# Optimization experiments

Hardware: AMD Instinct MI355X
Metric: run time of the kernel (lower is better)

Reference implementation:

```python
import jax, jax.numpy as jnp
import numpy as np
import math

B, S, E = 4, 2048, 1024


def setup_inputs() -> dict:
    key = jax.random.key(0)
    ks = jax.random.split(key, 7)
    w_scale = 1.0 / math.sqrt(E)
    x = jax.random.normal(ks[0], (B, S, E), dtype=jnp.float32)
    Wq = jax.random.normal(ks[1], (E, E), dtype=jnp.float32) * w_scale
    bq = jax.random.normal(ks[2], (E,), dtype=jnp.float32) * 0.01
    Wk = jax.random.normal(ks[3], (E, E), dtype=jnp.float32) * w_scale
    bk = jax.random.normal(ks[4], (E,), dtype=jnp.float32) * 0.01
    Wv = jax.random.normal(ks[5], (E, E), dtype=jnp.float32) * w_scale
    bv = jax.random.normal(ks[6], (E,), dtype=jnp.float32) * 0.01
    # causal mask: True = attend, False = masked (mask == 0 -> -inf)
    mask = jnp.broadcast_to(jnp.tril(jnp.ones((S, S), dtype=bool)), (B, S, S))
    return {"x": x, "Wq": Wq, "bq": bq, "Wk": Wk, "bk": bk, "Wv": Wv, "bv": bv, "mask": mask}


def reference(x, Wq, bq, Wk, bk, Wv, bv, mask):
    # nn.Linear stores weight as [out, in]: y = x @ W.T + b
    Q = jnp.einsum("bse,oe->bso", x, Wq) + bq
    K = jnp.einsum("bse,oe->bso", x, Wk) + bk
    V = jnp.einsum("bse,oe->bso", x, Wv) + bv
    scale = math.sqrt(E)
    scores = jnp.einsum("bqe,bke->bqk", Q, K) / scale  # [B,S,S]
    scores = jnp.where(mask, scores, -jnp.inf)
    attn = jax.nn.softmax(scores, axis=-1)
    out = jnp.einsum("bqk,bke->bqe", attn, V)  # [B,S,E]
    return out
```

## Files before the change

kernel.cpp:

```cpp
#include <hip/hip_runtime.h>
#include <stdint.h>

typedef unsigned short u16;
typedef __attribute__((ext_vector_type(8))) short bf16x8;
typedef __attribute__((ext_vector_type(4))) float f32x4;

#define MFMA16(a, b, c) __builtin_amdgcn_mfma_f32_16x16x32_bf16((a), (b), (c), 0, 0, 0)

#define MASKVAL (-1.0e30f)

#define WAITV(N) asm volatile("s_waitcnt vmcnt(" #N ")" ::: "memory")
#define LGKM0()  asm volatile("s_waitcnt lgkmcnt(0)" ::: "memory")
#define SBAR()   __builtin_amdgcn_s_barrier()

__device__ __forceinline__ u16 f2bf(float f) {
  union { float f; uint32_t u; } v; v.f = f;
  uint32_t u = v.u;
  u += 0x7fffu + ((u >> 16) & 1u);
  return (u16)(u >> 16);
}
__device__ __forceinline__ void async16(const void* g, void* l) {
  __builtin_amdgcn_global_load_lds(
      (const __attribute__((address_space(1))) unsigned int*)g,
      (__attribute__((address_space(3))) unsigned int*)l, 16, 0, 0);
}

__global__ __launch_bounds__(256) void conv_kernel(
    const float* __restrict__ x,  const float* __restrict__ wq,
    const float* __restrict__ wk, const float* __restrict__ wv,
    u16* __restrict__ xb, u16* __restrict__ wb, int do_wv)
{
  const int NX = 1 << 20;
  const int NW = 1 << 17;
  const int total = NX + NW * (do_wv ? 3 : 2);
  for (int i = blockIdx.x * 256 + threadIdx.x; i < total; i += gridDim.x * 256) {
    const float* src; u16* dst;
    if (i < NX) {
      src = x + (size_t)i * 8;
      const int m = i >> 7, k8 = i & 127;
      dst = xb + (size_t)m * 2048 + 1024 + k8 * 8;
    } else {
      const int j = i - NX;
      const int wsel = j >> 17;
      const int jj = j & (NW - 1);
      const float* W = (wsel == 0) ? wq : (wsel == 1) ? wk : wv;
      const int zoff = (wsel == 0) ? 0 : (wsel == 1) ? (2 << 20) : (1 << 20);
      src = W + (size_t)jj * 8;
      dst = wb + zoff + jj * 8;
    }
    float4 f0 = *(const float4*)src;
    float4 f1 = *(const float4*)(src + 4);
    ushort4 h0, h1;
    h0.x = f2bf(f0.x); h0.y = f2bf(f0.y); h0.z = f2bf(f0.z); h0.w = f2bf(f0.w);
    h1.x = f2bf(f1.x); h1.y = f2bf(f1.y); h1.z = f2bf(f1.z); h1.w = f2bf(f1.w);
    *(ushort4*)dst = h0;
    *(ushort4*)(dst + 4) = h1;
  }
}

template <int BMODE>
__global__ __launch_bounds__(256) void gemm_kernel(
    const u16* __restrict__ xb,
    const u16* __restrict__ wb,
    const float* __restrict__ wv_f,
    const float* __restrict__ bq, const float* __restrict__ bk,
    const float* __restrict__ bv,
    u16* __restrict__ q_out, u16* __restrict__ vt_out, u16* __restrict__ k_out,
    int mode)
{
  __shared__ u16 lA[2][128 * 32];
  __shared__ u16 lB[2][128 * 32];

  const int flat = blockIdx.x;
  const int xcd = flat & 7, idx = flat >> 3;
  int n_g, mm, z;
  if (mode == 0)      { n_g = xcd * 3 + idx % 3;  mm = idx / 3;  z = n_g >> 3; }
  else if (mode == 1) { n_g = xcd * 2 + (idx & 1); mm = idx >> 1; z = (n_g < 8) ? 0 : 2; }
  else                { n_g = xcd;                 mm = idx;      z = 1; }
  const int m0 = mm * 128, n0 = (n_g & 7) * 128;

  const int tid = threadIdx.x, lane = tid & 63, w = tid >> 6;
  const int quad = lane >> 4, l15 = lane & 15;
  const int wr = (w >> 1) * 64, wc = (w & 1) * 64;

  const u16* wz = wb + ((size_t)z << 20);
  const float* bias = (z == 0) ? bq : (z == 1) ? bv : bk;

  const int sr  = lane >> 2;
  const int ssw = (lane >> 3) & 3;
  const int c16s = (lane & 3) ^ ssw;

  auto stageA = [&](int kk, int bbuf) {
    const int k0 = kk * 32;
#pragma unroll
    for (int i = 0; i < 2; ++i) {
      const int r = w * 32 + i * 16 + sr;
      async16(&xb[(size_t)(m0 + r) * 2048 + 1024 + k0 + c16s * 8],
              &lA[bbuf][w * 1024 + i * 512]);
    }
  };
  auto stageB = [&](int kk, int bbuf) {
    const int k0 = kk * 32;
#pragma unroll
    for (int i = 0; i < 2; ++i) {
      const int r = w * 32 + i * 16 + sr;
      async16(&wz[(size_t)(n0 + r) * 1024 + k0 + c16s * 8],
              &lB[bbuf][w * 1024 + i * 512]);
    }
  };

  float4 bfr[4];
  const int br = tid >> 1;
  const int bcb = (tid & 1) * 2;
  const int bs = (br >> 1) & 3;
  auto loadB = [&](int kk) {
    const float* p = &wv_f[(size_t)(n0 + br) * 1024 + kk * 32 + bcb * 8];
    bfr[0] = ((const float4*)p)[0];
    bfr[1] = ((const float4*)p)[1];
    bfr[2] = ((const float4*)p)[2];
    bfr[3] = ((const float4*)p)[3];
  };
  auto writeB = [&](int bbuf) {
    ushort4 h[4];
#pragma unroll
    for (int g = 0; g < 4; ++g) {
      h[g].x = f2bf(bfr[g].x); h[g].y = f2bf(bfr[g].y);
      h[g].z = f2bf(bfr[g].z); h[g].w = f2bf(bfr[g].w);
    }
    const int p0 = (bcb + 0) ^ bs, p1 = (bcb + 1) ^ bs;
    *(ushort4*)&lB[bbuf][br * 32 + p0 * 8]     = h[0];
    *(ushort4*)&lB[bbuf][br * 32 + p0 * 8 + 4] = h[1];
    *(ushort4*)&lB[bbuf][br * 32 + p1 * 8]     = h[2];
    *(ushort4*)&lB[bbuf][br * 32 + p1 * 8 + 4] = h[3];
  };

  f32x4 zero4 = {0.f, 0.f, 0.f, 0.f};
  f32x4 acc[4][4];
#pragma unroll
  for (int i = 0; i < 4; ++i)
#pragma unroll
    for (int j = 0; j < 4; ++j) acc[i][j] = zero4;

  if constexpr (BMODE == 0) {
    stageA(0, 0); stageB(0, 0);
  } else {
    stageA(0, 0); loadB(0); writeB(0);
  }

  const int fxor = (l15 >> 1) & 3;
  for (int kk = 0; kk < 32; ++kk) {
    const int bbuf = kk & 1;
    __syncthreads();
    if (kk + 1 < 32) {
      stageA(kk + 1, bbuf ^ 1);
      if constexpr (BMODE == 0) stageB(kk + 1, bbuf ^ 1);
      else loadB(kk + 1);
    }
    bf16x8 af[4], bw[4];
#pragma unroll
    for (int mf = 0; mf < 4; ++mf)
      af[mf] = *(const bf16x8*)
          &lA[bbuf][(wr + mf * 16 + l15) * 32 + (quad ^ fxor) * 8];
#pragma unroll
    for (int nf = 0; nf < 4; ++nf)
      bw[nf] = *(const bf16x8*)
          &lB[bbuf][(wc + nf * 16 + l15) * 32 + (quad ^ fxor) * 8];
    __builtin_amdgcn_s_setprio(1);
#pragma unroll
    for (int mf = 0; mf < 4; ++mf)
#pragma unroll
      for (int nf = 0; nf < 4; ++nf)
        acc[mf][nf] = MFMA16(af[mf], bw[nf], acc[mf][nf]);
    __builtin_amdgcn_s_setprio(0);
    if constexpr (BMODE == 1) {
      if (kk + 1 < 32) writeB(bbuf ^ 1);
    }
  }

  float bvv[4];
#pragma unroll
  for (int nf = 0; nf < 4; ++nf)
    bvv[nf] = bias[n0 + wc + nf * 16 + l15];

  if (z == 0) {
    const float qs = 0.03125f;
#pragma unroll
    for (int mf = 0; mf < 4; ++mf) {
#pragma unroll
      for (int nf = 0; nf < 4; ++nf) {
        const int n = n0 + wc + nf * 16 + l15;
#pragma unroll
        for (int r = 0; r < 4; ++r) {
          const int m = m0 + wr + mf * 16 + quad * 4 + r;
          q_out[(size_t)m * 2048 + n] = f2bf((acc[mf][nf][r] + bvv[nf]) * qs);
        }
      }
    }
  } else if (z == 1) {
#pragma unroll
    for (int mf = 0; mf < 4; ++mf) {
      const int mbase = m0 + wr + mf * 16 + quad * 4;
      const int bb = mbase >> 11;
      const int ss = mbase & 2047;
#pragma unroll
      for (int nf = 0; nf < 4; ++nf) {
        const int n = n0 + wc + nf * 16 + l15;
        ushort4 pk;
        pk.x = f2bf(acc[mf][nf][0] + bvv[nf]);
        pk.y = f2bf(acc[mf][nf][1] + bvv[nf]);
        pk.z = f2bf(acc[mf][nf][2] + bvv[nf]);
        pk.w = f2bf(acc[mf][nf][3] + bvv[nf]);
        *(ushort4*)&vt_out[((size_t)bb << 21) + (size_t)n * 2048 + ss] = pk;
      }
    }
  } else {
#pragma unroll
    for (int mf = 0; mf < 4; ++mf) {
#pragma unroll
      for (int nf = 0; nf < 4; ++nf) {
        const int n = n0 + wc + nf * 16 + l15;
#pragma unroll
        for (int r = 0; r < 4; ++r) {
          const int m = m0 + wr + mf * 16 + quad * 4 + r;
          k_out[(size_t)m * 1024 + n] = f2bf(acc[mf][nf][r] + bvv[nf]);
        }
      }
    }
  }
}

__global__ __launch_bounds__(512) void attn_kernel(
    const u16* __restrict__ Q, const u16* __restrict__ K,
    const u16* __restrict__ VT, float* out)
{
  constexpr int SLOT = 20480;
  __shared__ u16   ring[3][SLOT];
  __shared__ float sS[32 * 132];
  __shared__ u16   sP[32 * 136];
  __shared__ float sAlpha[32];
  __shared__ float sLinv[32];

  const int lin = blockIdx.x + ((int)blockIdx.y << 6);
  const int xcd = lin & 7;
  const int t = ((lin >> 3) << 1) | (xcd & 1);
  const int b = xcd >> 1;
  const int q0 = t * 32;
  const int tid = threadIdx.x, lane = tid & 63, w = tid >> 6;
  const int quad = lane >> 4, l15 = lane & 15;
  const u16* Qb  = Q  + ((size_t)b << 22);
  const u16* Kb  = K  + ((size_t)b << 21);
  const u16* VTb = VT + ((size_t)b << 21);
  float* outb = out + ((size_t)b << 21);

  const int sr = lane >> 4;
  const int sp = lane & 15;

  auto issueK = [&](int kv0, int e0, u16* slot) {
#pragma unroll
    for (int jj = 0; jj < 4; ++jj) {
      const int j = w * 4 + jj;
      const int r = j * 4 + sr;
      const int c16 = sp ^ (r & 15);
      async16(&Kb[(size_t)(kv0 + r) * 1024 + e0 + c16 * 8], slot + j * 512);
    }
  };
  auto issueV = [&](int kv0, int ck, u16* slot) {
#pragma unroll
    for (int jj = 0; jj < 4; ++jj) {
      const int j = w * 4 + jj;
      const int r = j * 4 + sr;
      const int c16 = sp ^ (r & 15);
      async16(&VTb[(size_t)(ck * 128 + r) * 2048 + kv0 + c16 * 8], slot + j * 512);
    }
  };
  auto issueQ = [&](int cq, u16* slot) {
    const int r = w * 4 + sr;
    const int c16 = sp ^ (r & 15);
    async16(&Qb[(size_t)(q0 + r) * 2048 + cq * 128 + c16 * 8],
            slot + 16384 + w * 512);
  };

  f32x4 zero4 = {0.f, 0.f, 0.f, 0.f};
  f32x4 accO[8][2];
#pragma unroll
  for (int c = 0; c < 8; ++c)
#pragma unroll
    for (int i = 0; i < 2; ++i) accO[c][i] = zero4;

  float m_i = MASKVAL, l_i = 0.f;
  const int srow = tid >> 4, slane = tid & 15;

  issueK(0, 0, ring[0]);   issueQ(0, ring[0]);
  issueK(0, 128, ring[1]); issueQ(1, ring[1]);
  int sl = 0, sl2 = 2;

  const int niter = q0 / 128 + 1;
  for (int it = 0; it < niter; ++it) {
    const int kv0 = it * 128;

    f32x4 accS[2];
    accS[0] = zero4; accS[1] = zero4;

#pragma unroll
    for (int c = 0; c < 8; ++c) {
      if (c < 7) { WAITV(5); } else { WAITV(4); }
      SBAR();
      u16* dst = ring[sl2];
      if (c < 6)      { issueK(kv0, (c + 2) * 128, dst); issueQ(c + 2, dst); }
      else if (c == 6) issueV(kv0, 0, dst);
      else             issueV(kv0, 1, dst);
      const u16* bufK = ring[sl];
      const u16* bufQ = ring[sl] + 16384;
      __builtin_amdgcn_s_setprio(1);
#pragma unroll
      for (int ks = 0; ks < 4; ++ks) {
        const int cc = ks * 4 + quad;
        bf16x8 a0 = *(const bf16x8*)&bufQ[l15 * 128 + (cc ^ l15) * 8];
        bf16x8 a1 = *(const bf16x8*)&bufQ[(16 + l15) * 128 + (cc ^ l15) * 8];
        bf16x8 b0 = *(const bf16x8*)&bufK[(w * 16 + l15) * 128 + (cc ^ l15) * 8];
        accS[0] = MFMA16(a0, b0, accS[0]);
        accS[1] = MFMA16(a1, b0, accS[1]);
      }
      __builtin_amdgcn_s_setprio(0);
      sl  = (sl  == 2) ? 0 : sl  + 1;
      sl2 = (sl2 == 2) ? 0 : sl2 + 1;
    }

#pragma unroll
    for (int mf = 0; mf < 2; ++mf)
#pragma unroll
      for (int r = 0; r < 4; ++r) {
        const int row = mf * 16 + quad * 4 + r;
        const int col = w * 16 + l15;
        sS[row * 132 + col] = (kv0 + col <= q0 + row) ? accS[mf][r] : MASKVAL;
      }
    LGKM0();
    SBAR();

    {
      float v[8];
      float4 t0 = *(const float4*)&sS[srow * 132 + slane * 8 + 0];
      float4 t1 = *(const float4*)&sS[srow * 132 + slane * 8 + 4];
      v[0]=t0.x; v[1]=t0.y; v[2]=t0.z; v[3]=t0.w;
      v[4]=t1.x; v[5]=t1.y; v[6]=t1.z; v[7]=t1.w;
      float mx = v[0];
#pragma unroll
      for (int j = 1; j < 8; ++j) mx = fmaxf(mx, v[j]);
#pragma unroll
      for (int d = 1; d < 16; d <<= 1) mx = fmaxf(mx, __shfl_xor(mx, d, 64));
      const float mnew  = fmaxf(m_i, mx);
      const float alpha = __expf(m_i - mnew);
      float sum = 0.f;
      u16 pb[8];
#pragma unroll
      for (int j = 0; j < 8; ++j) {
        const float p = __expf(v[j] - mnew);
        pb[j] = f2bf(p);
        union { uint32_t u; float f; } pv; pv.u = ((uint32_t)pb[j]) << 16;
        sum += pv.f;
      }
      ushort4 pk0, pk1;
      pk0.x = pb[0]; pk0.y = pb[1]; pk0.z = pb[2]; pk0.w = pb[3];
      pk1.x = pb[4]; pk1.y = pb[5]; pk1.z = pb[6]; pk1.w = pb[7];
      *(ushort4*)&sP[srow * 136 + slane * 8 + 0] = pk0;
      *(ushort4*)&sP[srow * 136 + slane * 8 + 4] = pk1;
#pragma unroll
      for (int d = 1; d < 16; d <<= 1) sum += __shfl_xor(sum, d, 64);
      l_i = l_i * alpha + sum;
      m_i = mnew;
      if (slane == 0) sAlpha[srow] = alpha;
      if (it == niter - 1 && slane == 0) sLinv[srow] = 1.0f / l_i;
    }
    LGKM0();
    SBAR();

    float av[2][4];
#pragma unroll
    for (int mf = 0; mf < 2; ++mf)
#pragma unroll
      for (int r = 0; r < 4; ++r)
        av[mf][r] = sAlpha[mf * 16 + quad * 4 + r];
#pragma unroll
    for (int c = 0; c < 8; ++c)
#pragma unroll
      for (int mf = 0; mf < 2; ++mf)
#pragma unroll
        for (int r = 0; r < 4; ++r) accO[c][mf][r] *= av[mf][r];

    bf16x8 pf0[4], pf1[4];
#pragma unroll
    for (int ks = 0; ks < 4; ++ks) {
      const int cc = ks * 4 + quad;
      pf0[ks] = *(const bf16x8*)&sP[l15 * 136 + cc * 8];
      pf1[ks] = *(const bf16x8*)&sP[(16 + l15) * 136 + cc * 8];
    }

#pragma unroll
    for (int k = 0; k < 8; ++k) {
      if (k < 7)                 { WAITV(4); }
      else if (it + 1 < niter)   { WAITV(5); }
      else                       { WAITV(0); }
      SBAR();
      u16* dst = ring[sl2];
      if (k < 6) issueV(kv0, k + 2, dst);
      else if (it + 1 < niter) {
        issueK(kv0 + 128, (k - 6) * 128, dst);
        issueQ(k - 6, dst);
      }
      const u16* bufV = ring[sl];
      __builtin_amdgcn_s_setprio(1);
#pragma unroll
      for (int ks = 0; ks < 4; ++ks) {
        const int cc = ks * 4 + quad;
        bf16x8 v0 = *(const bf16x8*)&bufV[(w * 16 + l15) * 128 + (cc ^ l15) * 8];
        accO[k][0] = MFMA16(pf0[ks], v0, accO[k][0]);
        accO[k][1] = MFMA16(pf1[ks], v0, accO[k][1]);
      }
      __builtin_amdgcn_s_setprio(0);
      sl  = (sl  == 2) ? 0 : sl  + 1;
      sl2 = (sl2 == 2) ? 0 : sl2 + 1;
    }
  }

  float lv[2][4];
#pragma unroll
  for (int mf = 0; mf < 2; ++mf)
#pragma unroll
    for (int r = 0; r < 4; ++r)
      lv[mf][r] = sLinv[mf * 16 + quad * 4 + r];
#pragma unroll
  for (int c = 0; c < 8; ++c)
#pragma unroll
    for (int mf = 0; mf < 2; ++mf) {
      const int col = c * 128 + w * 16 + l15;
#pragma unroll
      for (int r = 0; r < 4; ++r) {
        const int row = q0 + mf * 16 + quad * 4 + r;
        outb[(size_t)row * 1024 + col] = accO[c][mf][r] * lv[mf][r];
      }
    }
}

extern "C" void kernel_launch(void* const* d_in, const int* in_sizes, int n_in,
                              void* d_out, int out_size, void* d_ws, size_t ws_size,
                              hipStream_t stream) {
  (void)in_sizes; (void)n_in; (void)out_size;
  const float* x  = (const float*)d_in[0];
  const float* Wq = (const float*)d_in[1];
  const float* bq = (const float*)d_in[2];
  const float* Wk = (const float*)d_in[3];
  const float* bk = (const float*)d_in[4];
  const float* Wv = (const float*)d_in[5];
  const float* bv = (const float*)d_in[6];

  u16* qbuf = (u16*)d_out;
  u16* vtw  = (u16*)d_in[7];
  u16* kw   = (u16*)d_ws;

  const bool ws_big = ws_size >= (size_t)22 * 1024 * 1024;
  u16* wb = ws_big ? (u16*)d_ws + (8u << 20) : (u16*)d_in[7];

  conv_kernel<<<dim3(2048), 256, 0, stream>>>(x, Wq, Wk, Wv, qbuf, wb,
                                              ws_big ? 1 : 0);
  if (ws_big) {
    gemm_kernel<0><<<dim3(1536), 256, 0, stream>>>(
        qbuf, wb, Wv, bq, bk, bv, qbuf, vtw, kw, 0);
  } else {
    gemm_kernel<0><<<dim3(1024), 256, 0, stream>>>(
        qbuf, wb, Wv, bq, bk, bv, qbuf, vtw, kw, 1);
    gemm_kernel<1><<<dim3(512), 256, 0, stream>>>(
        qbuf, wb, Wv, bq, bk, bv, qbuf, vtw, kw, 2);
  }

  attn_kernel<<<dim3(64, 4), 512, 0, stream>>>(qbuf, kw, vtw, (float*)d_out);
}
```

Before: 414.0 us.

## Enlarge attention query tile to 64 rows and triple-buffer projection GEMM

The attention kernel now processes 64 query rows per block instead of 32. It arranges 8 waves as a 2x4 grid, does the softmax in registers with cross-wave max/sum exchange through small shared arrays, and double-buffers Q in its own LDS area. This halves K/V reloads per query and removes the sS score staging, at the cost of more registers and fewer blocks (128 instead of 256 on a large GPU). The projection GEMM moves from double to triple-buffered async loads with explicit vmcnt waits, and the V path with inline fp32 conversion is split into its own kernel.

```diff
diff --git a/kernel.cpp b/kernel.cpp
--- a/kernel.cpp
+++ b/kernel.cpp
@@ -58,25 +58,22 @@
   }
 }
 
-template <int BMODE>
 __global__ __launch_bounds__(256) void gemm_kernel(
     const u16* __restrict__ xb,
     const u16* __restrict__ wb,
-    const float* __restrict__ wv_f,
     const float* __restrict__ bq, const float* __restrict__ bk,
     const float* __restrict__ bv,
     u16* __restrict__ q_out, u16* __restrict__ vt_out, u16* __restrict__ k_out,
     int mode)
 {
-  __shared__ u16 lA[2][128 * 32];
-  __shared__ u16 lB[2][128 * 32];
+  __shared__ u16 lA[3][128 * 32];
+  __shared__ u16 lB[3][128 * 32];
 
   const int flat = blockIdx.x;
   const int xcd = flat & 7, idx = flat >> 3;
   int n_g, mm, z;
   if (mode == 0)      { n_g = xcd * 3 + idx % 3;  mm = idx / 3;  z = n_g >> 3; }
-  else if (mode == 1) { n_g = xcd * 2 + (idx & 1); mm = idx >> 1; z = (n_g < 8) ? 0 : 2; }
-  else                { n_g = xcd;                 mm = idx;      z = 1; }
+  else                { n_g = xcd * 2 + (idx & 1); mm = idx >> 1; z = (n_g < 8) ? 0 : 2; }
   const int m0 = mm * 128, n0 = (n_g & 7) * 128;
 
   const int tid = threadIdx.x, lane = tid & 63, w = tid >> 6;
@@ -109,6 +106,125 @@
     }
   };
 
+  f32x4 zero4 = {0.f, 0.f, 0.f, 0.f};
+  f32x4 acc[4][4];
+#pragma unroll
+  for (int i = 0; i < 4; ++i)
+#pragma unroll
+    for (int j = 0; j < 4; ++j) acc[i][j] = zero4;
+
+  stageA(0, 0); stageB(0, 0);
+  stageA(1, 1); stageB(1, 1);
+
+  const int fxor = (l15 >> 1) & 3;
+  int cur = 0;
+  for (int kk = 0; kk < 32; ++kk) {
+    if (kk < 31) { WAITV(4); } else { WAITV(0); }
+    SBAR();
+    if (kk + 2 < 32) {
+      int nx = cur + 2; if (nx >= 3) nx -= 3;
+      stageA(kk + 2, nx);
+      stageB(kk + 2, nx);
+    }
+    bf16x8 af[4], bw[4];
+#pragma unroll
+    for (int mf = 0; mf < 4; ++mf)
+      af[mf] = *(const bf16x8*)
+          &lA[cur][(wr + mf * 16 + l15) * 32 + (quad ^ fxor) * 8];
+#pragma unroll
+    for (int nf = 0; nf < 4; ++nf)
+      bw[nf] = *(const bf16x8*)
+          &lB[cur][(wc + nf * 16 + l15) * 32 + (quad ^ fxor) * 8];
+    __builtin_amdgcn_s_setprio(1);
+#pragma unroll
+    for (int mf = 0; mf < 4; ++mf)
+#pragma unroll
+      for (int nf = 0; nf < 4; ++nf)
+        acc[mf][nf] = MFMA16(af[mf], bw[nf], acc[mf][nf]);
+    __builtin_amdgcn_s_setprio(0);
+    cur = (cur == 2) ? 0 : cur + 1;
+  }
+
+  float bvv[4];
+#pragma unroll
+  for (int nf = 0; nf < 4; ++nf)
+    bvv[nf] = bias[n0 + wc + nf * 16 + l15];
+
+  if (z == 0) {
+    const float qs = 0.03125f;
+#pragma unroll
+    for (int mf = 0; mf < 4; ++mf) {
+#pragma unroll
+      for (int nf = 0; nf < 4; ++nf) {
+        const int n = n0 + wc + nf * 16 + l15;
+#pragma unroll
+        for (int r = 0; r < 4; ++r) {
+          const int m = m0 + wr + mf * 16 + quad * 4 + r;
+          q_out[(size_t)m * 2048 + n] = f2bf((acc[mf][nf][r] + bvv[nf]) * qs);
+        }
+      }
+    }
+  } else if (z == 1) {
+#pragma unroll
+    for (int mf = 0; mf < 4; ++mf) {
+      const int mbase = m0 + wr + mf * 16 + quad * 4;
+      const int bb = mbase >> 11;
+      const int ss = mbase & 2047;
+#pragma unroll
+      for (int nf = 0; nf < 4; ++nf) {
+        const int n = n0 + wc + nf * 16 + l15;
+        ushort4 pk;
+        pk.x = f2bf(acc[mf][nf][0] + bvv[nf]);
+        pk.y = f2bf(acc[mf][nf][1] + bvv[nf]);
+        pk.z = f2bf(acc[mf][nf][2] + bvv[nf]);
+        pk.w = f2bf(acc[mf][nf][3] + bvv[nf]);
+        *(ushort4*)&vt_out[((size_t)bb << 21) + (size_t)n * 2048 + ss] = pk;
+      }
+    }
+  } else {
+#pragma unroll
+    for (int mf = 0; mf < 4; ++mf) {
+#pragma unroll
+      for (int nf = 0; nf < 4; ++nf) {
+        const int n = n0 + wc + nf * 16 + l15;
+#pragma unroll
+        for (int r = 0; r < 4; ++r) {
+          const int m = m0 + wr + mf * 16 + quad * 4 + r;
+          k_out[(size_t)m * 1024 + n] = f2bf(acc[mf][nf][r] + bvv[nf]);
+        }
+      }
+    }
+  }
+}
+
+__global__ __launch_bounds__(256) void gemm_v_kernel(
+    const u16* __restrict__ xb, const float* __restrict__ wv_f,
+    const float* __restrict__ bv, u16* __restrict__ vt_out)
+{
+  __shared__ u16 lA[2][128 * 32];
+  __shared__ u16 lB[2][128 * 32];
+
+  const int flat = blockIdx.x;
+  const int xcd = flat & 7, idx = flat >> 3;
+  const int m0 = idx * 128, n0 = xcd * 128;
+
+  const int tid = threadIdx.x, lane = tid & 63, w = tid >> 6;
+  const int quad = lane >> 4, l15 = lane & 15;
+  const int wr = (w >> 1) * 64, wc = (w & 1) * 64;
+
+  const int sr  = lane >> 2;
+  const int ssw = (lane >> 3) & 3;
+  const int c16s = (lane & 3) ^ ssw;
+
+  auto stageA = [&](int kk, int bbuf) {
+    const int k0 = kk * 32;
+#pragma unroll
+    for (int i = 0; i < 2; ++i) {
+      const int r = w * 32 + i * 16 + sr;
+      async16(&xb[(size_t)(m0 + r) * 2048 + 1024 + k0 + c16s * 8],
+              &lA[bbuf][w * 1024 + i * 512]);
+    }
+  };
   float4 bfr[4];
   const int br = tid >> 1;
   const int bcb = (tid & 1) * 2;
@@ -141,21 +257,13 @@
 #pragma unroll
     for (int j = 0; j < 4; ++j) acc[i][j] = zero4;
 
-  if constexpr (BMODE == 0) {
-    stageA(0, 0); stageB(0, 0);
-  } else {
-    stageA(0, 0); loadB(0); writeB(0);
-  }
+  stageA(0, 0); loadB(0); writeB(0);
 
   const int fxor = (l15 >> 1) & 3;
   for (int kk = 0; kk < 32; ++kk) {
     const int bbuf = kk & 1;
     __syncthreads();
-    if (kk + 1 < 32) {
-      stageA(kk + 1, bbuf ^ 1);
-      if constexpr (BMODE == 0) stageB(kk + 1, bbuf ^ 1);
-      else loadB(kk + 1);
-    }
+    if (kk + 1 < 32) { stageA(kk + 1, bbuf ^ 1); loadB(kk + 1); }
     bf16x8 af[4], bw[4];
 #pragma unroll
     for (int mf = 0; mf < 4; ++mf)
@@ -165,66 +273,32 @@
     for (int nf = 0; nf < 4; ++nf)
       bw[nf] = *(const bf16x8*)
           &lB[bbuf][(wc + nf * 16 + l15) * 32 + (quad ^ fxor) * 8];
-    __builtin_amdgcn_s_setprio(1);
 #pragma unroll
     for (int mf = 0; mf < 4; ++mf)
 #pragma unroll
       for (int nf = 0; nf < 4; ++nf)
         acc[mf][nf] = MFMA16(af[mf], bw[nf], acc[mf][nf]);
-    __builtin_amdgcn_s_setprio(0);
-    if constexpr (BMODE == 1) {
-      if (kk + 1 < 32) writeB(bbuf ^ 1);
-    }
+    if (kk + 1 < 32) writeB(bbuf ^ 1);
   }
 
   float bvv[4];
 #pragma unroll
   for (int nf = 0; nf < 4; ++nf)
-    bvv[nf] = bias[n0 + wc + nf * 16 + l15];
-
-  if (z == 0) {
-    const float qs = 0.03125f;
-#pragma unroll
-    for (int mf = 0; mf < 4; ++mf) {
-#pragma unroll
-      for (int nf = 0; nf < 4; ++nf) {
-        const int n = n0 + wc + nf * 16 + l15;
-#pragma unroll
-        for (int r = 0; r < 4; ++r) {
-          const int m = m0 + wr + mf * 16 + quad * 4 + r;
-          q_out[(size_t)m * 2048 + n] = f2bf((acc[mf][nf][r] + bvv[nf]) * qs);
-        }
-      }
-    }
-  } else if (z == 1) {
-#pragma unroll
-    for (int mf = 0; mf < 4; ++mf) {
-      const int mbase = m0 + wr + mf * 16 + quad * 4;
-      const int bb = mbase >> 11;
-      const int ss = mbase & 2047;
-#pragma unroll
-      for (int nf = 0; nf < 4; ++nf) {
-        const int n = n0 + wc + nf * 16 + l15;
-        ushort4 pk;
-        pk.x = f2bf(acc[mf][nf][0] + bvv[nf]);
-        pk.y = f2bf(acc[mf][nf][1] + bvv[nf]);
-        pk.z = f2bf(acc[mf][nf][2] + bvv[nf]);
-        pk.w = f2bf(acc[mf][nf][3] + bvv[nf]);
-        *(ushort4*)&vt_out[((size_t)bb << 21) + (size_t)n * 2048 + ss] = pk;
-      }
-    }
-  } else {
-#pragma unroll
-    for (int mf = 0; mf < 4; ++mf) {
-#pragma unroll
-      for (int nf = 0; nf < 4; ++nf) {
-        const int n = n0 + wc + nf * 16 + l15;
-#pragma unroll
-        for (int r = 0; r < 4; ++r) {
-          const int m = m0 + wr + mf * 16 + quad * 4 + r;
-          k_out[(size_t)m * 1024 + n] = f2bf(acc[mf][nf][r] + bvv[nf]);
-        }
-      }
+    bvv[nf] = bv[n0 + wc + nf * 16 + l15];
+#pragma unroll
+  for (int mf = 0; mf < 4; ++mf) {
+    const int mbase = m0 + wr + mf * 16 + quad * 4;
+    const int bb = mbase >> 11;
+    const int ss = mbase & 2047;
+#pragma unroll
+    for (int nf = 0; nf < 4; ++nf) {
+      const int n = n0 + wc + nf * 16 + l15;
+      ushort4 pk;
+      pk.x = f2bf(acc[mf][nf][0] + bvv[nf]);
+      pk.y = f2bf(acc[mf][nf][1] + bvv[nf]);
+      pk.z = f2bf(acc[mf][nf][2] + bvv[nf]);
+      pk.w = f2bf(acc[mf][nf][3] + bvv[nf]);
+      *(ushort4*)&vt_out[((size_t)bb << 21) + (size_t)n * 2048 + ss] = pk;
     }
   }
 }
@@ -233,20 +307,21 @@
     const u16* __restrict__ Q, const u16* __restrict__ K,
     const u16* __restrict__ VT, float* out)
 {
-  constexpr int SLOT = 20480;
-  __shared__ u16   ring[3][SLOT];
-  __shared__ float sS[32 * 132];
-  __shared__ u16   sP[32 * 136];
-  __shared__ float sAlpha[32];
-  __shared__ float sLinv[32];
-
-  const int lin = blockIdx.x + ((int)blockIdx.y << 6);
+  __shared__ u16   ring[3][16384];
+  __shared__ u16   qd[2][8192];
+  __shared__ u16   sP[64 * 136];
+  __shared__ float pmaxb[64][4];
+  __shared__ float psumb[64][4];
+
+  const int lin = blockIdx.x + ((int)blockIdx.y << 5);
   const int xcd = lin & 7;
   const int t = ((lin >> 3) << 1) | (xcd & 1);
   const int b = xcd >> 1;
-  const int q0 = t * 32;
+  const int q0 = t * 64;
   const int tid = threadIdx.x, lane = tid & 63, w = tid >> 6;
   const int quad = lane >> 4, l15 = lane & 15;
+  const int wq = w >> 2;
+  const int wk = w & 3;
   const u16* Qb  = Q  + ((size_t)b << 22);
   const u16* Kb  = K  + ((size_t)b << 21);
   const u16* VTb = VT + ((size_t)b << 21);
@@ -255,71 +330,88 @@
   const int sr = lane >> 4;
   const int sp = lane & 15;
 
-  auto issueK = [&](int kv0, int e0, u16* slot) {
+  auto issueK = [&](int kv0_, int e0, u16* slot) {
 #pragma unroll
     for (int jj = 0; jj < 4; ++jj) {
       const int j = w * 4 + jj;
       const int r = j * 4 + sr;
       const int c16 = sp ^ (r & 15);
-      async16(&Kb[(size_t)(kv0 + r) * 1024 + e0 + c16 * 8], slot + j * 512);
-    }
-  };
-  auto issueV = [&](int kv0, int ck, u16* slot) {
+      async16(&Kb[(size_t)(kv0_ + r) * 1024 + e0 + c16 * 8], slot + j * 512);
+    }
+  };
+  auto issueV = [&](int kv0_, int ck, u16* slot) {
 #pragma unroll
     for (int jj = 0; jj < 4; ++jj) {
       const int j = w * 4 + jj;
       const int r = j * 4 + sr;
       const int c16 = sp ^ (r & 15);
-      async16(&VTb[(size_t)(ck * 128 + r) * 2048 + kv0 + c16 * 8], slot + j * 512);
-    }
-  };
-  auto issueQ = [&](int cq, u16* slot) {
-    const int r = w * 4 + sr;
-    const int c16 = sp ^ (r & 15);
-    async16(&Qb[(size_t)(q0 + r) * 2048 + cq * 128 + c16 * 8],
-            slot + 16384 + w * 512);
+      async16(&VTb[(size_t)(ck * 128 + r) * 2048 + kv0_ + c16 * 8], slot + j * 512);
+    }
+  };
+  auto issueQ = [&](int cq) {
+#pragma unroll
+    for (int jj = 0; jj < 2; ++jj) {
+      const int j = w * 2 + jj;
+      const int r = j * 4 + sr;
+      const int c16 = sp ^ (r & 15);
+      async16(&Qb[(size_t)(q0 + r) * 2048 + cq * 128 + c16 * 8],
+              &qd[cq & 1][j * 512]);
+    }
   };
 
   f32x4 zero4 = {0.f, 0.f, 0.f, 0.f};
-  f32x4 accO[8][2];
+  f32x4 accO[8][2][2];
 #pragma unroll
   for (int c = 0; c < 8; ++c)
 #pragma unroll
-    for (int i = 0; i < 2; ++i) accO[c][i] = zero4;
-
-  float m_i = MASKVAL, l_i = 0.f;
-  const int srow = tid >> 4, slane = tid & 15;
-
-  issueK(0, 0, ring[0]);   issueQ(0, ring[0]);
-  issueK(0, 128, ring[1]); issueQ(1, ring[1]);
+    for (int i = 0; i < 2; ++i)
+#pragma unroll
+      for (int j = 0; j < 2; ++j) accO[c][i][j] = zero4;
+
+  float m_i[2][4], l_i[2][4];
+#pragma unroll
+  for (int mf = 0; mf < 2; ++mf)
+#pragma unroll
+    for (int rr = 0; rr < 4; ++rr) { m_i[mf][rr] = MASKVAL; l_i[mf][rr] = 0.f; }
+
+  issueQ(0);
+  issueK(0, 0, ring[0]);
+  issueK(0, 128, ring[1]);
   int sl = 0, sl2 = 2;
 
   const int niter = q0 / 128 + 1;
   for (int it = 0; it < niter; ++it) {
     const int kv0 = it * 128;
 
-    f32x4 accS[2];
-    accS[0] = zero4; accS[1] = zero4;
+    f32x4 accS[2][2];
+#pragma unroll
+    for (int i = 0; i < 2; ++i)
+#pragma unroll
+      for (int j = 0; j < 2; ++j) accS[i][j] = zero4;
 
 #pragma unroll
     for (int c = 0; c < 8; ++c) {
-      if (c < 7) { WAITV(5); } else { WAITV(4); }
+      WAITV(4);
       SBAR();
+      issueQ((c + 1) & 7);
       u16* dst = ring[sl2];
-      if (c < 6)      { issueK(kv0, (c + 2) * 128, dst); issueQ(c + 2, dst); }
+      if (c < 6)       issueK(kv0, (c + 2) * 128, dst);
       else if (c == 6) issueV(kv0, 0, dst);
       else             issueV(kv0, 1, dst);
       const u16* bufK = ring[sl];
-      const u16* bufQ = ring[sl] + 16384;
+      const u16* bufQ = qd[c & 1];
       __builtin_amdgcn_s_setprio(1);
 #pragma unroll
       for (int ks = 0; ks < 4; ++ks) {
         const int cc = ks * 4 + quad;
-        bf16x8 a0 = *(const bf16x8*)&bufQ[l15 * 128 + (cc ^ l15) * 8];
-        bf16x8 a1 = *(const bf16x8*)&bufQ[(16 + l15) * 128 + (cc ^ l15) * 8];
-        bf16x8 b0 = *(const bf16x8*)&bufK[(w * 16 + l15) * 128 + (cc ^ l15) * 8];
-        accS[0] = MFMA16(a0, b0, accS[0]);
-        accS[1] = MFMA16(a1, b0, accS[1]);
+        bf16x8 a0 = *(const bf16x8*)&bufQ[(wq * 32 + l15) * 128 + (cc ^ l15) * 8];
+        bf16x8 a1 = *(const bf16x8*)&bufQ[(wq * 32 + 16 + l15) * 128 + (cc ^ l15) * 8];
+        bf16x8 b0 = *(const bf16x8*)&bufK[(wk * 32 + l15) * 128 + (cc ^ l15) * 8];
+        bf16x8 b1 = *(const bf16x8*)&bufK[(wk * 32 + 16 + l15) * 128 + (cc ^ l15) * 8];
+        accS[0][0] = MFMA16(a0, b0, accS[0][0]);
+        accS[0][1] = MFMA16(a0, b1, accS[0][1]);
+        accS[1][0] = MFMA16(a1, b0, accS[1][0]);
+        accS[1][1] = MFMA16(a1, b1, accS[1][1]);
       }
       __builtin_amdgcn_s_setprio(0);
       sl  = (sl  == 2) ? 0 : sl  + 1;
@@ -329,92 +421,88 @@
 #pragma unroll
     for (int mf = 0; mf < 2; ++mf)
 #pragma unroll
-      for (int r = 0; r < 4; ++r) {
-        const int row = mf * 16 + quad * 4 + r;
-        const int col = w * 16 + l15;
-        sS[row * 132 + col] = (kv0 + col <= q0 + row) ? accS[mf][r] : MASKVAL;
+      for (int rr = 0; rr < 4; ++rr) {
+        const int R = wq * 32 + mf * 16 + quad * 4 + rr;
+        const int gr = q0 + R;
+        const float s0 = (kv0 + wk * 32 + l15      <= gr) ? accS[mf][0][rr] : MASKVAL;
+        const float s1 = (kv0 + wk * 32 + 16 + l15 <= gr) ? accS[mf][1][rr] : MASKVAL;
+        float m = fmaxf(s0, s1);
+#pragma unroll
+        for (int d = 1; d < 16; d <<= 1) m = fmaxf(m, __shfl_xor(m, d, 64));
+        if (l15 == 0) pmaxb[R][wk] = m;
       }
     LGKM0();
     SBAR();
 
-    {
-      float v[8];
-      float4 t0 = *(const float4*)&sS[srow * 132 + slane * 8 + 0];
-      float4 t1 = *(const float4*)&sS[srow * 132 + slane * 8 + 4];
-      v[0]=t0.x; v[1]=t0.y; v[2]=t0.z; v[3]=t0.w;
-      v[4]=t1.x; v[5]=t1.y; v[6]=t1.z; v[7]=t1.w;
-      float mx = v[0];
-#pragma unroll
-      for (int j = 1; j < 8; ++j) mx = fmaxf(mx, v[j]);
-#pragma unroll
-      for (int d = 1; d < 16; d <<= 1) mx = fmaxf(mx, __shfl_xor(mx, d, 64));
-      const float mnew  = fmaxf(m_i, mx);
-      const float alpha = __expf(m_i - mnew);
-      float sum = 0.f;
-      u16 pb[8];
-#pragma unroll
-      for (int j = 0; j < 8; ++j) {
-        const float p = __expf(v[j] - mnew);
-        pb[j] = f2bf(p);
-        union { uint32_t u; float f; } pv; pv.u = ((uint32_t)pb[j]) << 16;
-        sum += pv.f;
-      }
-      ushort4 pk0, pk1;
-      pk0.x = pb[0]; pk0.y = pb[1]; pk0.z = pb[2]; pk0.w = pb[3];
-      pk1.x = pb[4]; pk1.y = pb[5]; pk1.z = pb[6]; pk1.w = pb[7];
-      *(ushort4*)&sP[srow * 136 + slane * 8 + 0] = pk0;
-      *(ushort4*)&sP[srow * 136 + slane * 8 + 4] = pk1;
-#pragma unroll
-      for (int d = 1; d < 16; d <<= 1) sum += __shfl_xor(sum, d, 64);
-      l_i = l_i * alpha + sum;
-      m_i = mnew;
-      if (slane == 0) sAlpha[srow] = alpha;
-      if (it == niter - 1 && slane == 0) sLinv[srow] = 1.0f / l_i;
-    }
+    float alpha_[2][4];
+#pragma unroll
+    for (int mf = 0; mf < 2; ++mf)
+#pragma unroll
+      for (int rr = 0; rr < 4; ++rr) {
+        const int R = wq * 32 + mf * 16 + quad * 4 + rr;
+        const int gr = q0 + R;
+        const float4 pm4 = *(const float4*)&pmaxb[R][0];
+        const float mrow = fmaxf(fmaxf(pm4.x, pm4.y), fmaxf(pm4.z, pm4.w));
+        const float mnew = fmaxf(m_i[mf][rr], mrow);
+        alpha_[mf][rr] = __expf(m_i[mf][rr] - mnew);
+        m_i[mf][rr] = mnew;
+        float s = 0.f;
+#pragma unroll
+        for (int nf = 0; nf < 2; ++nf) {
+          const int C = wk * 32 + nf * 16 + l15;
+          const float p = (kv0 + C <= gr) ? __expf(accS[mf][nf][rr] - mnew) : 0.f;
+          const u16 pb = f2bf(p);
+          sP[R * 136 + C] = pb;
+          union { uint32_t u; float f; } pv; pv.u = ((uint32_t)pb) << 16;
+          s += pv.f;
+        }
+#pragma unroll
+        for (int d = 1; d < 16; d <<= 1) s += __shfl_xor(s, d, 64);
+        if (l15 == 0) psumb[R][wk] = s;
+      }
     LGKM0();
     SBAR();
 
-    float av[2][4];
 #pragma unroll
     for (int mf = 0; mf < 2; ++mf)
 #pragma unroll
-      for (int r = 0; r < 4; ++r)
-        av[mf][r] = sAlpha[mf * 16 + quad * 4 + r];
-#pragma unroll
-    for (int c = 0; c < 8; ++c)
+      for (int rr = 0; rr < 4; ++rr) {
+        const int R = wq * 32 + mf * 16 + quad * 4 + rr;
+        const float4 ps4 = *(const float4*)&psumb[R][0];
+        l_i[mf][rr] = l_i[mf][rr] * alpha_[mf][rr] + (ps4.x + ps4.y + ps4.z + ps4.w);
+      }
+#pragma unroll
+    for (int cA = 0; cA < 8; ++cA)
 #pragma unroll
       for (int mf = 0; mf < 2; ++mf)
 #pragma unroll
-        for (int r = 0; r < 4; ++r) accO[c][mf][r] *= av[mf][r];
-
-    bf16x8 pf0[4], pf1[4];
-#pragma unroll
-    for (int ks = 0; ks < 4; ++ks) {
-      const int cc = ks * 4 + quad;
-      pf0[ks] = *(const bf16x8*)&sP[l15 * 136 + cc * 8];
-      pf1[ks] = *(const bf16x8*)&sP[(16 + l15) * 136 + cc * 8];
-    }
+        for (int nf = 0; nf < 2; ++nf)
+#pragma unroll
+          for (int rr = 0; rr < 4; ++rr)
+            accO[cA][mf][nf][rr] *= alpha_[mf][rr];
 
 #pragma unroll
     for (int k = 0; k < 8; ++k) {
-      if (k < 7)                 { WAITV(4); }
-      else if (it + 1 < niter)   { WAITV(5); }
-      else                       { WAITV(0); }
+      if (k == 0)                          { WAITV(6); }
+      else if (k < 7 || it + 1 < niter)    { WAITV(4); }
+      else                                 { WAITV(0); }
       SBAR();
       u16* dst = ring[sl2];
       if (k < 6) issueV(kv0, k + 2, dst);
-      else if (it + 1 < niter) {
-        issueK(kv0 + 128, (k - 6) * 128, dst);
-        issueQ(k - 6, dst);
-      }
+      else if (it + 1 < niter) issueK(kv0 + 128, (k - 6) * 128, dst);
       const u16* bufV = ring[sl];
       __builtin_amdgcn_s_setprio(1);
 #pragma unroll
       for (int ks = 0; ks < 4; ++ks) {
         const int cc = ks * 4 + quad;
-        bf16x8 v0 = *(const bf16x8*)&bufV[(w * 16 + l15) * 128 + (cc ^ l15) * 8];
-        accO[k][0] = MFMA16(pf0[ks], v0, accO[k][0]);
-        accO[k][1] = MFMA16(pf1[ks], v0, accO[k][1]);
+        bf16x8 p0 = *(const bf16x8*)&sP[(wq * 32 + l15) * 136 + cc * 8];
+        bf16x8 p1 = *(const bf16x8*)&sP[(wq * 32 + 16 + l15) * 136 + cc * 8];
+        bf16x8 v0 = *(const bf16x8*)&bufV[(wk * 32 + l15) * 128 + (cc ^ l15) * 8];
+        bf16x8 v1 = *(const bf16x8*)&bufV[(wk * 32 + 16 + l15) * 128 + (cc ^ l15) * 8];
+        accO[k][0][0] = MFMA16(p0, v0, accO[k][0][0]);
+        accO[k][0][1] = MFMA16(p0, v1, accO[k][0][1]);
+        accO[k][1][0] = MFMA16(p1, v0, accO[k][1][0]);
+        accO[k][1][1] = MFMA16(p1, v1, accO[k][1][1]);
       }
       __builtin_amdgcn_s_setprio(0);
       sl  = (sl  == 2) ? 0 : sl  + 1;
@@ -422,23 +510,24 @@
     }
   }
 
-  float lv[2][4];
+  float linv[2][4];
 #pragma unroll
   for (int mf = 0; mf < 2; ++mf)
 #pragma unroll
-    for (int r = 0; r < 4; ++r)
-      lv[mf][r] = sLinv[mf * 16 + quad * 4 + r];
+    for (int rr = 0; rr < 4; ++rr) linv[mf][rr] = 1.0f / l_i[mf][rr];
 #pragma unroll
   for (int c = 0; c < 8; ++c)
 #pragma unroll
-    for (int mf = 0; mf < 2; ++mf) {
-      const int col = c * 128 + w * 16 + l15;
-#pragma unroll
-      for (int r = 0; r < 4; ++r) {
-        const int row = q0 + mf * 16 + quad * 4 + r;
-        outb[(size_t)row * 1024 + col] = accO[c][mf][r] * lv[mf][r];
-      }
-    }
+    for (int mf = 0; mf < 2; ++mf)
+#pragma unroll
+      for (int nf = 0; nf < 2; ++nf) {
+        const int col = c * 128 + wk * 32 + nf * 16 + l15;
+#pragma unroll
+        for (int rr = 0; rr < 4; ++rr) {
+          const int row = q0 + wq * 32 + mf * 16 + quad * 4 + rr;
+          outb[(size_t)row * 1024 + col] = accO[c][mf][nf][rr] * linv[mf][rr];
+        }
+      }
 }
 
 extern "C" void kernel_launch(void* const* d_in, const int* in_sizes, int n_in,
@@ -463,14 +552,13 @@
   conv_kernel<<<dim3(2048), 256, 0, stream>>>(x, Wq, Wk, Wv, qbuf, wb,
                                               ws_big ? 1 : 0);
   if (ws_big) {
-    gemm_kernel<0><<<dim3(1536), 256, 0, stream>>>(
-        qbuf, wb, Wv, bq, bk, bv, qbuf, vtw, kw, 0);
+    gemm_kernel<<<dim3(1536), 256, 0, stream>>>(
+        qbuf, wb, bq, bk, bv, qbuf, vtw, kw, 0);
   } else {
-    gemm_kernel<0><<<dim3(1024), 256, 0, stream>>>(
-        qbuf, wb, Wv, bq, bk, bv, qbuf, vtw, kw, 1);
-    gemm_kernel<1><<<dim3(512), 256, 0, stream>>>(
-        qbuf, wb, Wv, bq, bk, bv, qbuf, vtw, kw, 2);
-  }
-
-  attn_kernel<<<dim3(64, 4), 512, 0, stream>>>(qbuf, kw, vtw, (float*)d_out);
-}
+    gemm_kernel<<<dim3(1024), 256, 0, stream>>>(
+        qbuf, wb, bq, bk, bv, qbuf, vtw, kw, 1);
+    gemm_v_kernel<<<dim3(512), 256, 0, stream>>>(qbuf, Wv, bv, vtw);
+  }
+
+  attn_kernel<<<dim3(32, 4), 512, 0, stream>>>(qbuf, kw, vtw, (float*)d_out);
+}
```

New measurement: 691.5 us. 1.67x slower.

## Replace QKV projection GEMM with 256x256-tile 8-wave ping-pong pipelined kernel

Applied to the files above, without the earlier changes.

The 128x128 tile, 4-wave QKV GEMM is replaced by a 512-thread kernel. It computes 256x256 output tiles with a K step of 64 and double-buffered half-tiles in LDS. Global-to-LDS async loads are interleaved with MFMA phases under barriers and explicit vmcnt waits. The larger tile raises arithmetic intensity and cuts block count, at the cost of more registers and LDS, fewer blocks per CU, and wave-quantization risk. The small-workspace fallback keeps a separate V GEMM kernel that converts Wv on the fly.

```diff
diff --git a/kernel.cpp b/kernel.cpp
--- a/kernel.cpp
+++ b/kernel.cpp
@@ -58,33 +58,292 @@
   }
 }
 
-template <int BMODE>
-__global__ __launch_bounds__(256) void gemm_kernel(
+__global__ __launch_bounds__(512) void gemm8_kernel(
     const u16* __restrict__ xb,
     const u16* __restrict__ wb,
-    const float* __restrict__ wv_f,
     const float* __restrict__ bq, const float* __restrict__ bk,
     const float* __restrict__ bv,
     u16* __restrict__ q_out, u16* __restrict__ vt_out, u16* __restrict__ k_out,
-    int mode)
+    int np)
+{
+  __shared__ u16 lA[2][2][128 * 64];
+  __shared__ u16 lB[2][2][128 * 64];
+
+  const int flat = blockIdx.x;
+  const int xcd = flat & 7, idx = flat >> 3;
+  int n_g, mm;
+  if (np == 12) { n_g = (xcd & 3) * 3 + idx % 3; mm = (xcd >> 2) * 16 + idx / 3; }
+  else          { n_g = xcd;                     mm = idx; }
+  const int z = (np == 12) ? (n_g >> 2) : ((n_g >> 2) ? 2 : 0);
+  const int m0 = mm * 256;
+  const int n0loc = (n_g & 3) * 256;
+  const u16* wz = wb + ((size_t)z << 20);
+  const float* bias = (z == 0) ? bq : (z == 1) ? bv : bk;
+
+  const int tid = threadIdx.x, lane = tid & 63, w = tid >> 6;
+  const int quad = lane >> 4, l15 = lane & 15;
+  const int wm = w >> 2, wn = w & 3;
+
+  const int srow = lane >> 3;
+  const int schk = (lane & 7) ^ srow;
+
+  auto stageA = [&](int d, int h, int kt) {
+#pragma unroll
+    for (int i = 0; i < 2; ++i) {
+      const int rr = w * 16 + i * 8;
+      async16(&xb[(size_t)(m0 + h * 128 + rr + srow) * 2048 + 1024 + kt * 64 + schk * 8],
+              &lA[d][h][rr * 64]);
+    }
+  };
+  auto stageB = [&](int d, int h, int kt) {
+#pragma unroll
+    for (int i = 0; i < 2; ++i) {
+      const int rr = w * 16 + i * 8;
+      async16(&wz[(size_t)(n0loc + h * 128 + rr + srow) * 1024 + kt * 64 + schk * 8],
+              &lB[d][h][rr * 64]);
+    }
+  };
+
+  f32x4 zero4 = {0.f, 0.f, 0.f, 0.f};
+  f32x4 acc[8][4];
+#pragma unroll
+  for (int i = 0; i < 8; ++i)
+#pragma unroll
+    for (int j = 0; j < 4; ++j) acc[i][j] = zero4;
+
+  auto rdA = [&](int d, int mf, int ks) -> bf16x8 {
+    const int hr = mf * 16 + l15;
+    return *(const bf16x8*)&lA[d][wm][hr * 64 + (((ks << 2) + quad) ^ (l15 & 7)) * 8];
+  };
+  auto rdB = [&](int d, int nf, int ks) -> bf16x8 {
+    const int hr = (wn & 1) * 64 + nf * 16 + l15;
+    return *(const bf16x8*)&lB[d][wn >> 1][hr * 64 + (((ks << 2) + quad) ^ (l15 & 7)) * 8];
+  };
+
+  stageA(0, 0, 0); stageA(0, 1, 0);
+  stageB(0, 0, 0); stageB(0, 1, 0);
+  stageA(1, 0, 1); stageB(1, 1, 1);
+  WAITV(0);
+  SBAR();
+
+  bf16x8 a[4][2], b[2][2];
+  for (int i = 0; i < 8; ++i) {
+    const int k1 = 2 * i + 1, k2 = 2 * i + 2, k3 = 2 * i + 3;
+    const bool more = (i < 7);
+
+#pragma unroll
+    for (int mf = 0; mf < 4; ++mf)
+#pragma unroll
+      for (int ks = 0; ks < 2; ++ks) a[mf][ks] = rdA(0, mf, ks);
+#pragma unroll
+    for (int nf = 0; nf < 2; ++nf)
+#pragma unroll
+      for (int ks = 0; ks < 2; ++ks) b[nf][ks] = rdB(0, nf, ks);
+    stageA(1, 1, k1);
+    SBAR();
+    __builtin_amdgcn_s_setprio(1);
+#pragma unroll
+    for (int mf = 0; mf < 4; ++mf)
+#pragma unroll
+      for (int nf = 0; nf < 2; ++nf)
+#pragma unroll
+        for (int ks = 0; ks < 2; ++ks)
+          acc[mf][nf] = MFMA16(a[mf][ks], b[nf][ks], acc[mf][nf]);
+    __builtin_amdgcn_s_setprio(0);
+    SBAR();
+
+#pragma unroll
+    for (int nf = 0; nf < 2; ++nf)
+#pragma unroll
+      for (int ks = 0; ks < 2; ++ks) b[nf][ks] = rdB(0, 2 + nf, ks);
+    stageB(1, 0, k1);
+    SBAR();
+    __builtin_amdgcn_s_setprio(1);
+#pragma unroll
+    for (int mf = 0; mf < 4; ++mf)
+#pragma unroll
+      for (int nf = 0; nf < 2; ++nf)
+#pragma unroll
+        for (int ks = 0; ks < 2; ++ks)
+          acc[mf][2 + nf] = MFMA16(a[mf][ks], b[nf][ks], acc[mf][2 + nf]);
+    __builtin_amdgcn_s_setprio(0);
+    SBAR();
+
+#pragma unroll
+    for (int mf = 0; mf < 4; ++mf)
+#pragma unroll
+      for (int ks = 0; ks < 2; ++ks) a[mf][ks] = rdA(0, 4 + mf, ks);
+    if (more) stageA(0, 0, k2);
+    SBAR();
+    __builtin_amdgcn_s_setprio(1);
+#pragma unroll
+    for (int mf = 0; mf < 4; ++mf)
+#pragma unroll
+      for (int nf = 0; nf < 2; ++nf)
+#pragma unroll
+        for (int ks = 0; ks < 2; ++ks)
+          acc[4 + mf][2 + nf] = MFMA16(a[mf][ks], b[nf][ks], acc[4 + mf][2 + nf]);
+    __builtin_amdgcn_s_setprio(0);
+    SBAR();
+
+#pragma unroll
+    for (int nf = 0; nf < 2; ++nf)
+#pragma unroll
+      for (int ks = 0; ks < 2; ++ks) b[nf][ks] = rdB(0, nf, ks);
+    if (more) stageB(0, 1, k2);
+    SBAR();
+    __builtin_amdgcn_s_setprio(1);
+#pragma unroll
+    for (int mf = 0; mf < 4; ++mf)
+#pragma unroll
+      for (int nf = 0; nf < 2; ++nf)
+#pragma unroll
+        for (int ks = 0; ks < 2; ++ks)
+          acc[4 + mf][nf] = MFMA16(a[mf][ks], b[nf][ks], acc[4 + mf][nf]);
+    __builtin_amdgcn_s_setprio(0);
+    if (more) { WAITV(4); } else { WAITV(0); }
+    SBAR();
+
+#pragma unroll
+    for (int mf = 0; mf < 4; ++mf)
+#pragma unroll
+      for (int ks = 0; ks < 2; ++ks) a[mf][ks] = rdA(1, mf, ks);
+#pragma unroll
+    for (int nf = 0; nf < 2; ++nf)
+#pragma unroll
+      for (int ks = 0; ks < 2; ++ks) b[nf][ks] = rdB(1, nf, ks);
+    if (more) stageA(0, 1, k2);
+    SBAR();
+    __builtin_amdgcn_s_setprio(1);
+#pragma unroll
+    for (int mf = 0; mf < 4; ++mf)
+#pragma unroll
+      for (int nf = 0; nf < 2; ++nf)
+#pragma unroll
+        for (int ks = 0; ks < 2; ++ks)
+          acc[mf][nf] = MFMA16(a[mf][ks], b[nf][ks], acc[mf][nf]);
+    __builtin_amdgcn_s_setprio(0);
+    SBAR();
+
+#pragma unroll
+    for (int nf = 0; nf < 2; ++nf)
+#pragma unroll
+      for (int ks = 0; ks < 2; ++ks) b[nf][ks] = rdB(1, 2 + nf, ks);
+    if (more) stageB(0, 0, k2);
+    SBAR();
+    __builtin_amdgcn_s_setprio(1);
+#pragma unroll
+    for (int mf = 0; mf < 4; ++mf)
+#pragma unroll
+      for (int nf = 0; nf < 2; ++nf)
+#pragma unroll
+        for (int ks = 0; ks < 2; ++ks)
+          acc[mf][2 + nf] = MFMA16(a[mf][ks], b[nf][ks], acc[mf][2 + nf]);
+    __builtin_amdgcn_s_setprio(0);
+    SBAR();
+
+#pragma unroll
+    for (int mf = 0; mf < 4; ++mf)
+#pragma unroll
+      for (int ks = 0; ks < 2; ++ks) a[mf][ks] = rdA(1, 4 + mf, ks);
+    if (more) stageA(1, 0, k3);
+    SBAR();
+    __builtin_amdgcn_s_setprio(1);
+#pragma unroll
+    for (int mf = 0; mf < 4; ++mf)
+#pragma unroll
+      for (int nf = 0; nf < 2; ++nf)
+#pragma unroll
+        for (int ks = 0; ks < 2; ++ks)
+          acc[4 + mf][2 + nf] = MFMA16(a[mf][ks], b[nf][ks], acc[4 + mf][2 + nf]);
+    __builtin_amdgcn_s_setprio(0);
+    SBAR();
+
+#pragma unroll
+    for (int nf = 0; nf < 2; ++nf)
+#pragma unroll
+      for (int ks = 0; ks < 2; ++ks) b[nf][ks] = rdB(1, nf, ks);
+    if (more) stageB(1, 1, k3);
+    SBAR();
+    __builtin_amdgcn_s_setprio(1);
+#pragma unroll
+    for (int mf = 0; mf < 4; ++mf)
+#pragma unroll
+      for (int nf = 0; nf < 2; ++nf)
+#pragma unroll
+        for (int ks = 0; ks < 2; ++ks)
+          acc[4 + mf][nf] = MFMA16(a[mf][ks], b[nf][ks], acc[4 + mf][nf]);
+    __builtin_amdgcn_s_setprio(0);
+    if (more) { WAITV(4); }
+    SBAR();
+  }
+
+  float bvv[4];
+#pragma unroll
+  for (int nf = 0; nf < 4; ++nf)
+    bvv[nf] = bias[n0loc + wn * 64 + nf * 16 + l15];
+
+  if (z == 0) {
+    const float qs = 0.03125f;
+#pragma unroll
+    for (int mf = 0; mf < 8; ++mf) {
+#pragma unroll
+      for (int nf = 0; nf < 4; ++nf) {
+        const int n = n0loc + wn * 64 + nf * 16 + l15;
+#pragma unroll
+        for (int rr = 0; rr < 4; ++rr) {
+          const int m = m0 + wm * 128 + mf * 16 + quad * 4 + rr;
+          q_out[(size_t)m * 2048 + n] = f2bf((acc[mf][nf][rr] + bvv[nf]) * qs);
+        }
+      }
+    }
+  } else if (z == 1) {
+#pragma unroll
+    for (int mf = 0; mf < 8; ++mf) {
+      const int mbase = m0 + wm * 128 + mf * 16 + quad * 4;
+      const int bb = mbase >> 11;
+      const int ss = mbase & 2047;
+#pragma unroll
+      for (int nf = 0; nf < 4; ++nf) {
+        const int n = n0loc + wn * 64 + nf * 16 + l15;
+        ushort4 pk;
+        pk.x = f2bf(acc[mf][nf][0] + bvv[nf]);
+        pk.y = f2bf(acc[mf][nf][1] + bvv[nf]);
+        pk.z = f2bf(acc[mf][nf][2] + bvv[nf]);
+        pk.w = f2bf(acc[mf][nf][3] + bvv[nf]);
+        *(ushort4*)&vt_out[((size_t)bb << 21) + (size_t)n * 2048 + ss] = pk;
+      }
+    }
+  } else {
+#pragma unroll
+    for (int mf = 0; mf < 8; ++mf) {
+#pragma unroll
+      for (int nf = 0; nf < 4; ++nf) {
+        const int n = n0loc + wn * 64 + nf * 16 + l15;
+#pragma unroll
+        for (int rr = 0; rr < 4; ++rr) {
+          const int m = m0 + wm * 128 + mf * 16 + quad * 4 + rr;
+          k_out[(size_t)m * 1024 + n] = f2bf(acc[mf][nf][rr] + bvv[nf]);
+        }
+      }
+    }
+  }
+}
+
+__global__ __launch_bounds__(256) void gemm_v_kernel(
+    const u16* __restrict__ xb, const float* __restrict__ wv_f,
+    const float* __restrict__ bv, u16* __restrict__ vt_out)
 {
   __shared__ u16 lA[2][128 * 32];
   __shared__ u16 lB[2][128 * 32];
 
   const int flat = blockIdx.x;
   const int xcd = flat & 7, idx = flat >> 3;
-  int n_g, mm, z;
-  if (mode == 0)      { n_g = xcd * 3 + idx % 3;  mm = idx / 3;  z = n_g >> 3; }
-  else if (mode == 1) { n_g = xcd * 2 + (idx & 1); mm = idx >> 1; z = (n_g < 8) ? 0 : 2; }
-  else                { n_g = xcd;                 mm = idx;      z = 1; }
-  const int m0 = mm * 128, n0 = (n_g & 7) * 128;
+  const int m0 = idx * 128, n0 = xcd * 128;
 
   const int tid = threadIdx.x, lane = tid & 63, w = tid >> 6;
   const int quad = lane >> 4, l15 = lane & 15;
   const int wr = (w >> 1) * 64, wc = (w & 1) * 64;
-
-  const u16* wz = wb + ((size_t)z << 20);
-  const float* bias = (z == 0) ? bq : (z == 1) ? bv : bk;
 
   const int sr  = lane >> 2;
   const int ssw = (lane >> 3) & 3;
@@ -99,16 +358,6 @@
               &lA[bbuf][w * 1024 + i * 512]);
     }
   };
-  auto stageB = [&](int kk, int bbuf) {
-    const int k0 = kk * 32;
-#pragma unroll
-    for (int i = 0; i < 2; ++i) {
-      const int r = w * 32 + i * 16 + sr;
-      async16(&wz[(size_t)(n0 + r) * 1024 + k0 + c16s * 8],
-              &lB[bbuf][w * 1024 + i * 512]);
-    }
-  };
-
   float4 bfr[4];
   const int br = tid >> 1;
   const int bcb = (tid & 1) * 2;
@@ -141,21 +390,13 @@
 #pragma unroll
     for (int j = 0; j < 4; ++j) acc[i][j] = zero4;
 
-  if constexpr (BMODE == 0) {
-    stageA(0, 0); stageB(0, 0);
-  } else {
-    stageA(0, 0); loadB(0); writeB(0);
-  }
+  stageA(0, 0); loadB(0); writeB(0);
 
   const int fxor = (l15 >> 1) & 3;
   for (int kk = 0; kk < 32; ++kk) {
     const int bbuf = kk & 1;
     __syncthreads();
-    if (kk + 1 < 32) {
-      stageA(kk + 1, bbuf ^ 1);
-      if constexpr (BMODE == 0) stageB(kk + 1, bbuf ^ 1);
-      else loadB(kk + 1);
-    }
+    if (kk + 1 < 32) { stageA(kk + 1, bbuf ^ 1); loadB(kk + 1); }
     bf16x8 af[4], bw[4];
 #pragma unroll
     for (int mf = 0; mf < 4; ++mf)
@@ -165,66 +406,32 @@
     for (int nf = 0; nf < 4; ++nf)
       bw[nf] = *(const bf16x8*)
           &lB[bbuf][(wc + nf * 16 + l15) * 32 + (quad ^ fxor) * 8];
-    __builtin_amdgcn_s_setprio(1);
 #pragma unroll
     for (int mf = 0; mf < 4; ++mf)
 #pragma unroll
       for (int nf = 0; nf < 4; ++nf)
         acc[mf][nf] = MFMA16(af[mf], bw[nf], acc[mf][nf]);
-    __builtin_amdgcn_s_setprio(0);
-    if constexpr (BMODE == 1) {
-      if (kk + 1 < 32) writeB(bbuf ^ 1);
-    }
+    if (kk + 1 < 32) writeB(bbuf ^ 1);
   }
 
   float bvv[4];
 #pragma unroll
   for (int nf = 0; nf < 4; ++nf)
-    bvv[nf] = bias[n0 + wc + nf * 16 + l15];
-
-  if (z == 0) {
-    const float qs = 0.03125f;
-#pragma unroll
-    for (int mf = 0; mf < 4; ++mf) {
-#pragma unroll
-      for (int nf = 0; nf < 4; ++nf) {
-        const int n = n0 + wc + nf * 16 + l15;
-#pragma unroll
-        for (int r = 0; r < 4; ++r) {
-          const int m = m0 + wr + mf * 16 + quad * 4 + r;
-          q_out[(size_t)m * 2048 + n] = f2bf((acc[mf][nf][r] + bvv[nf]) * qs);
-        }
-      }
-    }
-  } else if (z == 1) {
-#pragma unroll
-    for (int mf = 0; mf < 4; ++mf) {
-      const int mbase = m0 + wr + mf * 16 + quad * 4;
-      const int bb = mbase >> 11;
-      const int ss = mbase & 2047;
-#pragma unroll
-      for (int nf = 0; nf < 4; ++nf) {
-        const int n = n0 + wc + nf * 16 + l15;
-        ushort4 pk;
-        pk.x = f2bf(acc[mf][nf][0] + bvv[nf]);
-        pk.y = f2bf(acc[mf][nf][1] + bvv[nf]);
-        pk.z = f2bf(acc[mf][nf][2] + bvv[nf]);
-        pk.w = f2bf(acc[mf][nf][3] + bvv[nf]);
-        *(ushort4*)&vt_out[((size_t)bb << 21) + (size_t)n * 2048 + ss] = pk;
-      }
-    }
-  } else {
-#pragma unroll
-    for (int mf = 0; mf < 4; ++mf) {
-#pragma unroll
-      for (int nf = 0; nf < 4; ++nf) {
-        const int n = n0 + wc + nf * 16 + l15;
-#pragma unroll
-        for (int r = 0; r < 4; ++r) {
-          const int m = m0 + wr + mf * 16 + quad * 4 + r;
-          k_out[(size_t)m * 1024 + n] = f2bf(acc[mf][nf][r] + bvv[nf]);
-        }
-      }
+    bvv[nf] = bv[n0 + wc + nf * 16 + l15];
+#pragma unroll
+  for (int mf = 0; mf < 4; ++mf) {
+    const int mbase = m0 + wr + mf * 16 + quad * 4;
+    const int bb = mbase >> 11;
+    const int ss = mbase & 2047;
+#pragma unroll
+    for (int nf = 0; nf < 4; ++nf) {
+      const int n = n0 + wc + nf * 16 + l15;
+      ushort4 pk;
+      pk.x = f2bf(acc[mf][nf][0] + bvv[nf]);
+      pk.y = f2bf(acc[mf][nf][1] + bvv[nf]);
+      pk.z = f2bf(acc[mf][nf][2] + bvv[nf]);
+      pk.w = f2bf(acc[mf][nf][3] + bvv[nf]);
+      *(ushort4*)&vt_out[((size_t)bb << 21) + (size_t)n * 2048 + ss] = pk;
     }
   }
 }
@@ -463,13 +670,12 @@
   conv_kernel<<<dim3(2048), 256, 0, stream>>>(x, Wq, Wk, Wv, qbuf, wb,
                                               ws_big ? 1 : 0);
   if (ws_big) {
-    gemm_kernel<0><<<dim3(1536), 256, 0, stream>>>(
-        qbuf, wb, Wv, bq, bk, bv, qbuf, vtw, kw, 0);
+    gemm8_kernel<<<dim3(384), 512, 0, stream>>>(
+        qbuf, wb, bq, bk, bv, qbuf, vtw, kw, 12);
   } else {
-    gemm_kernel<0><<<dim3(1024), 256, 0, stream>>>(
-        qbuf, wb, Wv, bq, bk, bv, qbuf, vtw, kw, 1);
-    gemm_kernel<1><<<dim3(512), 256, 0, stream>>>(
-        qbuf, wb, Wv, bq, bk, bv, qbuf, vtw, kw, 2);
+    gemm8_kernel<<<dim3(256), 512, 0, stream>>>(
+        qbuf, wb, bq, bk, bv, qbuf, vtw, kw, 8);
+    gemm_v_kernel<<<dim3(512), 256, 0, stream>>>(qbuf, Wv, bv, vtw);
   }
 
   attn_kernel<<<dim3(64, 4), 512, 0, stream>>>(qbuf, kw, vtw, (float*)d_out);
```

Result: no change. 416.2 us (+0.5%).
